# Kernel tuning notes

Measured on AMD Instinct MI355X. Metric: run time of the kernel, lower is better.

Reference implementation:

```python
import jax, jax.numpy as jnp
import numpy as np

GAMMA = 0.1
B, C, H, W = 8, 64, 64, 64
CINT = C // 8


def setup_inputs() -> dict:
    key = jax.random.key(0)
    ks = jax.random.split(key, 5)
    x = jax.random.normal(ks[0], (B, C, H, W), dtype=jnp.float32)
    Wq = jax.random.normal(ks[1], (CINT, C), dtype=jnp.float32) * 0.05
    Wk = jax.random.normal(ks[2], (CINT, C), dtype=jnp.float32) * 0.05
    Wv = jax.random.normal(ks[3], (CINT, C), dtype=jnp.float32) * 0.05
    Wout = jax.random.normal(ks[4], (C, CINT), dtype=jnp.float32) * 0.05
    return {"x": x, "Wq": Wq, "Wk": Wk, "Wv": Wv, "Wout": Wout}


def reference(x, Wq, Wk, Wv, Wout):
    b, c, h, w = x.shape
    n = h * w
    cint = Wq.shape[0]
    xf = x.reshape(b, c, n)                               # [B,C,N]
    q = jnp.einsum('ic,bcn->bin', Wq, xf)                 # [B,Cint,N]
    k = jnp.einsum('ic,bcn->bin', Wk, xf)
    v = jnp.einsum('ic,bcn->bin', Wv, xf)
    # scores[b, n, m] = q[b,:,n] . k[b,:,m]; softmax over dim=1 (the n axis)
    scores = jnp.einsum('bin,bim->bnm', q, k) / jnp.sqrt(jnp.asarray(cint, x.dtype))
    att = jax.nn.softmax(scores, axis=1)                  # [B,N,N], softmax over rows
    att_out = jnp.einsum('bin,bnm->bim', v, att)          # [B,Cint,N]
    out = jnp.einsum('ci,bim->bcm', Wout, att_out)        # [B,C,N]
    return x + out.reshape(b, c, h, w) * GAMMA
```

## Files before the change

### kernel.cpp

```cpp
#include <hip/hip_runtime.h>
#include <math.h>

#define BB 8
#define CC 64
#define NN 4096
#define CI 8
#define GAMMA 0.1f
#define SCALE (1.44269504088896f * 0.35355339059327f)
#define NSPLIT 4

typedef float v4f __attribute__((ext_vector_type(4)));
typedef __bf16 bf16x8 __attribute__((ext_vector_type(8)));
typedef __bf16 bf16x4 __attribute__((ext_vector_type(4)));

__device__ __forceinline__ float fast_exp2(float x) {
    return __builtin_amdgcn_exp2f(x);
}

__global__ __launch_bounds__(256) void qkv_kernel(
        const float* __restrict__ x,
        const float* __restrict__ Wq, const float* __restrict__ Wk,
        const float* __restrict__ Wv,
        __bf16* __restrict__ qbh, __bf16* __restrict__ kbh,
        __bf16* __restrict__ vbh, float* __restrict__ attab) {
    __shared__ float sw[3 * CI * CC];
    __shared__ unsigned short sq[32 * 8];
    __shared__ unsigned short sk[32 * 8];
    const int t = threadIdx.x;
    const int i  = t >> 5;
    const int nl = t & 31;
    const int b  = blockIdx.y;
    const int n0 = blockIdx.x * 32;

    for (int idx = t; idx < CI * CC; idx += 256) {
        sw[idx]                = Wq[idx];
        sw[CI * CC + idx]      = Wk[idx] * SCALE;
        sw[2 * CI * CC + idx]  = Wv[idx];
    }
    int lin = (blockIdx.y * (NN / 32) + blockIdx.x) * 256 + t;
    for (int idx = lin; idx < BB * 9 * NN; idx += BB * NN * CI) attab[idx] = 0.f;
    __syncthreads();

    const int n = n0 + nl;
    const float* xp = x + ((size_t)b * CC) * NN + n;
    const v4f* wq4 = (const v4f*)(sw + i * CC);
    const v4f* wk4 = (const v4f*)(sw + CI * CC + i * CC);
    const v4f* wv4 = (const v4f*)(sw + 2 * CI * CC + i * CC);
    float qa = 0.f, ka = 0.f, va = 0.f;
#pragma unroll 4
    for (int c4 = 0; c4 < CC / 4; ++c4) {
        v4f wq = wq4[c4], wk = wk4[c4], wv = wv4[c4];
        float x0 = xp[(size_t)(c4 * 4 + 0) * NN];
        float x1 = xp[(size_t)(c4 * 4 + 1) * NN];
        float x2 = xp[(size_t)(c4 * 4 + 2) * NN];
        float x3 = xp[(size_t)(c4 * 4 + 3) * NN];
        qa = fmaf(wq.x, x0, qa); ka = fmaf(wk.x, x0, ka); va = fmaf(wv.x, x0, va);
        qa = fmaf(wq.y, x1, qa); ka = fmaf(wk.y, x1, ka); va = fmaf(wv.y, x1, va);
        qa = fmaf(wq.z, x2, qa); ka = fmaf(wk.z, x2, ka); va = fmaf(wv.z, x2, va);
        qa = fmaf(wq.w, x3, qa); ka = fmaf(wk.w, x3, ka); va = fmaf(wv.w, x3, va);
    }
    __bf16 vb = (__bf16)va;
    vbh[((size_t)b * CI + i) * NN + n] = vb;
    __bf16 qb = (__bf16)qa, kb2 = (__bf16)ka;
    sq[nl * 8 + i] = *(unsigned short*)&qb;
    sk[nl * 8 + i] = *(unsigned short*)&kb2;
    __syncthreads();
    if (t < 32) {
        *(uint4*)(qbh + ((size_t)b * NN + n0 + t) * 8) = *(const uint4*)(sq + t * 8);
        *(uint4*)(kbh + ((size_t)b * NN + n0 + t) * 8) = *(const uint4*)(sk + t * 8);
    }
}

__global__ __launch_bounds__(256) void att_kernel(
        const __bf16* __restrict__ qbh, const __bf16* __restrict__ kbh,
        const __bf16* __restrict__ vbh, float* __restrict__ attab) {
    __shared__ unsigned short eld[4][2][16 * 36];
    const int t = threadIdx.x;
    const int w    = t >> 6;
    const int l    = t & 63;
    const int quad = l >> 4;
    const int lm   = l & 15;
    const int b  = blockIdx.z;
    const int m0 = blockIdx.x * 64 + w * 16;
    const int nbase = blockIdx.y * (NN / NSPLIT);
    const int HALF = (NN / NSPLIT) / 2;

    bf16x8 zero8, ones8;
#pragma unroll
    for (int z = 0; z < 8; ++z) { zero8[z] = (__bf16)0.0f; ones8[z] = (__bf16)1.0f; }

    bf16x8 kfrag = zero8;
    if (quad == 0)
        kfrag = *(const bf16x8*)(kbh + ((size_t)b * NN + m0 + lm) * 8);

    const __bf16* vrow = vbh + ((size_t)b * CI + (lm & 7)) * NN;
    const __bf16* qrow = qbh + (size_t)b * NN * 8;

    v4f acc0 = {0.f, 0.f, 0.f, 0.f};
    v4f acc1 = {0.f, 0.f, 0.f, 0.f};
    unsigned short* ew0 = &eld[w][0][lm * 36];
    unsigned short* ew1 = &eld[w][1][lm * 36];

    for (int ch = 0; ch < HALF / 32; ++ch) {
        const int nc0 = nbase + ch * 32;
        const int nc1 = nc0 + HALF;

        bf16x8 a_q0 = zero8, a_q1 = zero8;
        if (quad == 0) {
            a_q0 = *(const bf16x8*)(qrow + (size_t)(nc0 + lm) * 8);
            a_q1 = *(const bf16x8*)(qrow + (size_t)(nc0 + 16 + lm) * 8);
        }
        bf16x8 vf0;
        if (lm < 8)       vf0 = *(const bf16x8*)(vrow + nc0 + quad * 8);
        else if (lm == 8) vf0 = ones8;
        else              vf0 = zero8;
        v4f a_s0 = __builtin_amdgcn_mfma_f32_16x16x32_bf16(a_q0, kfrag, (v4f){0.f,0.f,0.f,0.f}, 0, 0, 0);
        v4f a_s1 = __builtin_amdgcn_mfma_f32_16x16x32_bf16(a_q1, kfrag, (v4f){0.f,0.f,0.f,0.f}, 0, 0, 0);

        bf16x8 b_q0 = zero8, b_q1 = zero8;
        if (quad == 0) {
            b_q0 = *(const bf16x8*)(qrow + (size_t)(nc1 + lm) * 8);
            b_q1 = *(const bf16x8*)(qrow + (size_t)(nc1 + 16 + lm) * 8);
        }
        bf16x8 vf1;
        if (lm < 8)       vf1 = *(const bf16x8*)(vrow + nc1 + quad * 8);
        else if (lm == 8) vf1 = ones8;
        else              vf1 = zero8;
        v4f b_s0 = __builtin_amdgcn_mfma_f32_16x16x32_bf16(b_q0, kfrag, (v4f){0.f,0.f,0.f,0.f}, 0, 0, 0);
        v4f b_s1 = __builtin_amdgcn_mfma_f32_16x16x32_bf16(b_q1, kfrag, (v4f){0.f,0.f,0.f,0.f}, 0, 0, 0);

        bf16x4 e;
        e[0] = (__bf16)fast_exp2(a_s0.x); e[1] = (__bf16)fast_exp2(a_s0.y);
        e[2] = (__bf16)fast_exp2(a_s0.z); e[3] = (__bf16)fast_exp2(a_s0.w);
        *(bf16x4*)(ew0 + quad * 4) = e;
        e[0] = (__bf16)fast_exp2(a_s1.x); e[1] = (__bf16)fast_exp2(a_s1.y);
        e[2] = (__bf16)fast_exp2(a_s1.z); e[3] = (__bf16)fast_exp2(a_s1.w);
        *(bf16x4*)(ew0 + 16 + quad * 4) = e;

        e[0] = (__bf16)fast_exp2(b_s0.x); e[1] = (__bf16)fast_exp2(b_s0.y);
        e[2] = (__bf16)fast_exp2(b_s0.z); e[3] = (__bf16)fast_exp2(b_s0.w);
        *(bf16x4*)(ew1 + quad * 4) = e;
        e[0] = (__bf16)fast_exp2(b_s1.x); e[1] = (__bf16)fast_exp2(b_s1.y);
        e[2] = (__bf16)fast_exp2(b_s1.z); e[3] = (__bf16)fast_exp2(b_s1.w);
        *(bf16x4*)(ew1 + 16 + quad * 4) = e;

        {
            bf16x4 lo = *(const bf16x4*)(ew0 + quad * 8);
            bf16x4 hi = *(const bf16x4*)(ew0 + quad * 8 + 4);
            bf16x8 ef;
#pragma unroll
            for (int z = 0; z < 4; ++z) { ef[z] = lo[z]; ef[4 + z] = hi[z]; }
            acc0 = __builtin_amdgcn_mfma_f32_16x16x32_bf16(vf0, ef, acc0, 0, 0, 0);
        }
        {
            bf16x4 lo = *(const bf16x4*)(ew1 + quad * 8);
            bf16x4 hi = *(const bf16x4*)(ew1 + quad * 8 + 4);
            bf16x8 ef;
#pragma unroll
            for (int z = 0; z < 4; ++z) { ef[z] = lo[z]; ef[4 + z] = hi[z]; }
            acc1 = __builtin_amdgcn_mfma_f32_16x16x32_bf16(vf1, ef, acc1, 0, 0, 0);
        }
    }

    v4f accO = {acc0.x + acc1.x, acc0.y + acc1.y, acc0.z + acc1.z, acc0.w + acc1.w};
    float* ap = attab + (size_t)b * 9 * NN + m0 + lm;
    float av[4] = {accO.x, accO.y, accO.z, accO.w};
#pragma unroll
    for (int r = 0; r < 4; ++r) {
        int i = quad * 4 + r;
        if (i < 9) atomicAdd(ap + (size_t)i * NN, av[r]);
    }
}

__global__ __launch_bounds__(256) void out_kernel(
        const float* __restrict__ x, const float* __restrict__ Wout,
        const float* __restrict__ attab, float* __restrict__ out) {
    const int t = threadIdx.x;
    const int c = blockIdx.y;
    const int b = blockIdx.z;
    const int m = (blockIdx.x * 256 + t) * 4;
    const float* ap = attab + (size_t)b * 9 * NN + m;
    v4f sum = *(const v4f*)(ap + (size_t)8 * NN);
    v4f s = {0.f, 0.f, 0.f, 0.f};
#pragma unroll
    for (int i = 0; i < CI; ++i) {
        float wgt = Wout[c * CI + i];
        v4f a = *(const v4f*)(ap + (size_t)i * NN);
        s.x = fmaf(wgt, a.x, s.x);
        s.y = fmaf(wgt, a.y, s.y);
        s.z = fmaf(wgt, a.z, s.z);
        s.w = fmaf(wgt, a.w, s.w);
    }
    size_t o = ((size_t)b * CC + c) * NN + m;
    v4f xv = *(const v4f*)(x + o);
    v4f r;
    r.x = xv.x + GAMMA * (s.x / sum.x);
    r.y = xv.y + GAMMA * (s.y / sum.y);
    r.z = xv.z + GAMMA * (s.z / sum.z);
    r.w = xv.w + GAMMA * (s.w / sum.w);
    *(v4f*)(out + o) = r;
}

extern "C" void kernel_launch(void* const* d_in, const int* in_sizes, int n_in,
                              void* d_out, int out_size, void* d_ws, size_t ws_size,
                              hipStream_t stream) {
    const float* x    = (const float*)d_in[0];
    const float* Wq   = (const float*)d_in[1];
    const float* Wk   = (const float*)d_in[2];
    const float* Wv   = (const float*)d_in[3];
    const float* Wout = (const float*)d_in[4];
    float* out = (float*)d_out;

    __bf16* qbh = (__bf16*)d_ws;
    __bf16* kbh = qbh + (size_t)BB * NN * 8;
    __bf16* vbh = kbh + (size_t)BB * NN * 8;
    float* attab = (float*)(vbh + (size_t)BB * NN * 8);

    qkv_kernel<<<dim3(NN / 32, BB), 256, 0, stream>>>(x, Wq, Wk, Wv, qbh, kbh, vbh, attab);
    att_kernel<<<dim3(NN / 64, NSPLIT, BB), 256, 0, stream>>>(qbh, kbh, vbh, attab);
    out_kernel<<<dim3(NN / 1024, CC, BB), 256, 0, stream>>>(x, Wout, attab, out);
}
```

Baseline: 113.8 us.

## Software-pipeline attention loop with prefetched Q/V and score MFMAs issued ahead

Restructures the att_kernel inner loop into a two-stage software pipeline. The Q and V fragments for the next 32-column chunk are loaded, and its score MFMAs issued, while the current chunk's exp2 and P·V MFMA run. The previous loop processed two interleaved halves with separate accumulators. The new loop walks chunks sequentially into one accumulator, which lengthens the MFMA dependency chain. The final prefetch reads past the split's range, harmlessly, into adjacent workspace.

Result: no change. 115.3 us (+1.3%).

```diff
diff --git a/kernel.cpp b/kernel.cpp
--- a/kernel.cpp
+++ b/kernel.cpp
@@ -83,7 +83,7 @@
     const int b  = blockIdx.z;
     const int m0 = blockIdx.x * 64 + w * 16;
     const int nbase = blockIdx.y * (NN / NSPLIT);
-    const int HALF = (NN / NSPLIT) / 2;
+    const int NCH = (NN / NSPLIT) / 32;
 
     bf16x8 zero8, ones8;
 #pragma unroll
@@ -93,56 +93,45 @@
     if (quad == 0)
         kfrag = *(const bf16x8*)(kbh + ((size_t)b * NN + m0 + lm) * 8);
 
+    const __bf16* qrow = qbh + (size_t)b * NN * 8;
     const __bf16* vrow = vbh + ((size_t)b * CI + (lm & 7)) * NN;
-    const __bf16* qrow = qbh + (size_t)b * NN * 8;
-
-    v4f acc0 = {0.f, 0.f, 0.f, 0.f};
-    v4f acc1 = {0.f, 0.f, 0.f, 0.f};
+    const bool q_on = (quad == 0);
+    const bool v_v  = (lm < 8);
+    const bool v_1  = (lm == 8);
+
     unsigned short* ew0 = &eld[w][0][lm * 36];
     unsigned short* ew1 = &eld[w][1][lm * 36];
 
-    for (int ch = 0; ch < HALF / 32; ++ch) {
-        const int nc0 = nbase + ch * 32;
-        const int nc1 = nc0 + HALF;
-
-        bf16x8 a_q0 = zero8, a_q1 = zero8;
-        if (quad == 0) {
-            a_q0 = *(const bf16x8*)(qrow + (size_t)(nc0 + lm) * 8);
-            a_q1 = *(const bf16x8*)(qrow + (size_t)(nc0 + 16 + lm) * 8);
-        }
-        bf16x8 vf0;
-        if (lm < 8)       vf0 = *(const bf16x8*)(vrow + nc0 + quad * 8);
-        else if (lm == 8) vf0 = ones8;
-        else              vf0 = zero8;
-        v4f a_s0 = __builtin_amdgcn_mfma_f32_16x16x32_bf16(a_q0, kfrag, (v4f){0.f,0.f,0.f,0.f}, 0, 0, 0);
-        v4f a_s1 = __builtin_amdgcn_mfma_f32_16x16x32_bf16(a_q1, kfrag, (v4f){0.f,0.f,0.f,0.f}, 0, 0, 0);
-
-        bf16x8 b_q0 = zero8, b_q1 = zero8;
-        if (quad == 0) {
-            b_q0 = *(const bf16x8*)(qrow + (size_t)(nc1 + lm) * 8);
-            b_q1 = *(const bf16x8*)(qrow + (size_t)(nc1 + 16 + lm) * 8);
-        }
-        bf16x8 vf1;
-        if (lm < 8)       vf1 = *(const bf16x8*)(vrow + nc1 + quad * 8);
-        else if (lm == 8) vf1 = ones8;
-        else              vf1 = zero8;
-        v4f b_s0 = __builtin_amdgcn_mfma_f32_16x16x32_bf16(b_q0, kfrag, (v4f){0.f,0.f,0.f,0.f}, 0, 0, 0);
-        v4f b_s1 = __builtin_amdgcn_mfma_f32_16x16x32_bf16(b_q1, kfrag, (v4f){0.f,0.f,0.f,0.f}, 0, 0, 0);
-
+    v4f accO = {0.f, 0.f, 0.f, 0.f};
+
+    bf16x8 q0a, q1a, va_, q0b, q1b, vb_;
+    {
+        const int nc = nbase;
+        q0a = q_on ? *(const bf16x8*)(qrow + (size_t)(nc + lm) * 8) : zero8;
+        q1a = q_on ? *(const bf16x8*)(qrow + (size_t)(nc + 16 + lm) * 8) : zero8;
+        va_ = v_v ? *(const bf16x8*)(vrow + nc + quad * 8) : (v_1 ? ones8 : zero8);
+    }
+    {
+        const int nc = nbase + 32;
+        q0b = q_on ? *(const bf16x8*)(qrow + (size_t)(nc + lm) * 8) : zero8;
+        q1b = q_on ? *(const bf16x8*)(qrow + (size_t)(nc + 16 + lm) * 8) : zero8;
+        vb_ = v_v ? *(const bf16x8*)(vrow + nc + quad * 8) : (v_1 ? ones8 : zero8);
+    }
+
+    v4f sc0 = __builtin_amdgcn_mfma_f32_16x16x32_bf16(q0a, kfrag, (v4f){0.f,0.f,0.f,0.f}, 0, 0, 0);
+    v4f sc1 = __builtin_amdgcn_mfma_f32_16x16x32_bf16(q1a, kfrag, (v4f){0.f,0.f,0.f,0.f}, 0, 0, 0);
+
+    for (int k = 0; k < NCH; k += 2) {
         bf16x4 e;
-        e[0] = (__bf16)fast_exp2(a_s0.x); e[1] = (__bf16)fast_exp2(a_s0.y);
-        e[2] = (__bf16)fast_exp2(a_s0.z); e[3] = (__bf16)fast_exp2(a_s0.w);
+        e[0] = (__bf16)fast_exp2(sc0.x); e[1] = (__bf16)fast_exp2(sc0.y);
+        e[2] = (__bf16)fast_exp2(sc0.z); e[3] = (__bf16)fast_exp2(sc0.w);
         *(bf16x4*)(ew0 + quad * 4) = e;
-        e[0] = (__bf16)fast_exp2(a_s1.x); e[1] = (__bf16)fast_exp2(a_s1.y);
-        e[2] = (__bf16)fast_exp2(a_s1.z); e[3] = (__bf16)fast_exp2(a_s1.w);
+        e[0] = (__bf16)fast_exp2(sc1.x); e[1] = (__bf16)fast_exp2(sc1.y);
+        e[2] = (__bf16)fast_exp2(sc1.z); e[3] = (__bf16)fast_exp2(sc1.w);
         *(bf16x4*)(ew0 + 16 + quad * 4) = e;
 
-        e[0] = (__bf16)fast_exp2(b_s0.x); e[1] = (__bf16)fast_exp2(b_s0.y);
-        e[2] = (__bf16)fast_exp2(b_s0.z); e[3] = (__bf16)fast_exp2(b_s0.w);
-        *(bf16x4*)(ew1 + quad * 4) = e;
-        e[0] = (__bf16)fast_exp2(b_s1.x); e[1] = (__bf16)fast_exp2(b_s1.y);
-        e[2] = (__bf16)fast_exp2(b_s1.z); e[3] = (__bf16)fast_exp2(b_s1.w);
-        *(bf16x4*)(ew1 + 16 + quad * 4) = e;
+        v4f t0 = __builtin_amdgcn_mfma_f32_16x16x32_bf16(q0b, kfrag, (v4f){0.f,0.f,0.f,0.f}, 0, 0, 0);
+        v4f t1 = __builtin_amdgcn_mfma_f32_16x16x32_bf16(q1b, kfrag, (v4f){0.f,0.f,0.f,0.f}, 0, 0, 0);
 
         {
             bf16x4 lo = *(const bf16x4*)(ew0 + quad * 8);
@@ -150,19 +139,43 @@
             bf16x8 ef;
 #pragma unroll
             for (int z = 0; z < 4; ++z) { ef[z] = lo[z]; ef[4 + z] = hi[z]; }
-            acc0 = __builtin_amdgcn_mfma_f32_16x16x32_bf16(vf0, ef, acc0, 0, 0, 0);
-        }
+            accO = __builtin_amdgcn_mfma_f32_16x16x32_bf16(va_, ef, accO, 0, 0, 0);
+        }
+        {
+            const int nc = nbase + (k + 2) * 32;
+            q0a = q_on ? *(const bf16x8*)(qrow + (size_t)(nc + lm) * 8) : zero8;
+            q1a = q_on ? *(const bf16x8*)(qrow + (size_t)(nc + 16 + lm) * 8) : zero8;
+            va_ = v_v ? *(const bf16x8*)(vrow + nc + quad * 8) : (v_1 ? ones8 : zero8);
+        }
+        sc0 = t0; sc1 = t1;
+
+        e[0] = (__bf16)fast_exp2(sc0.x); e[1] = (__bf16)fast_exp2(sc0.y);
+        e[2] = (__bf16)fast_exp2(sc0.z); e[3] = (__bf16)fast_exp2(sc0.w);
+        *(bf16x4*)(ew1 + quad * 4) = e;
+        e[0] = (__bf16)fast_exp2(sc1.x); e[1] = (__bf16)fast_exp2(sc1.y);
+        e[2] = (__bf16)fast_exp2(sc1.z); e[3] = (__bf16)fast_exp2(sc1.w);
+        *(bf16x4*)(ew1 + 16 + quad * 4) = e;
+
+        t0 = __builtin_amdgcn_mfma_f32_16x16x32_bf16(q0a, kfrag, (v4f){0.f,0.f,0.f,0.f}, 0, 0, 0);
+        t1 = __builtin_amdgcn_mfma_f32_16x16x32_bf16(q1a, kfrag, (v4f){0.f,0.f,0.f,0.f}, 0, 0, 0);
+
         {
             bf16x4 lo = *(const bf16x4*)(ew1 + quad * 8);
             bf16x4 hi = *(const bf16x4*)(ew1 + quad * 8 + 4);
             bf16x8 ef;
 #pragma unroll
             for (int z = 0; z < 4; ++z) { ef[z] = lo[z]; ef[4 + z] = hi[z]; }
-            acc1 = __builtin_amdgcn_mfma_f32_16x16x32_bf16(vf1, ef, acc1, 0, 0, 0);
-        }
-    }
-
-    v4f accO = {acc0.x + acc1.x, acc0.y + acc1.y, acc0.z + acc1.z, acc0.w + acc1.w};
+            accO = __builtin_amdgcn_mfma_f32_16x16x32_bf16(vb_, ef, accO, 0, 0, 0);
+        }
+        {
+            const int nc = nbase + (k + 3) * 32;
+            q0b = q_on ? *(const bf16x8*)(qrow + (size_t)(nc + lm) * 8) : zero8;
+            q1b = q_on ? *(const bf16x8*)(qrow + (size_t)(nc + 16 + lm) * 8) : zero8;
+            vb_ = v_v ? *(const bf16x8*)(vrow + nc + quad * 8) : (v_1 ? ones8 : zero8);
+        }
+        sc0 = t0; sc1 = t1;
+    }
+
     float* ap = attab + (size_t)b * 9 * NN + m0 + lm;
     float av[4] = {accO.x, accO.y, accO.z, accO.w};
 #pragma unroll
```
